# Performance work log

Hardware: AMD Instinct MI355X
Metric: run time of the kernel (lower is better)

## Reference

```python
import jax, jax.numpy as jnp
import numpy as np

N_ATOMS = 100000
BOX = 12.0
NS = 128            # 2**ceil(log2(2*(2*pi/mesh_spacing)*BOX/(2*pi) + 1)) with mesh_spacing=0.2
ORDER = 4           # interpolation_order (cubic)
SMEARING = 1.0      # atomic_gaussian_width
N_SPECIES = 2


def _weights_1d(x):
    # P3M order-4 assignment weights; offsets x in [-1/2, 1/2]
    x2 = x * x
    x3 = x2 * x
    return jnp.stack([
        (1.0 - 6.0 * x + 12.0 * x2 - 8.0 * x3) / 48.0,
        (23.0 - 30.0 * x - 12.0 * x2 + 24.0 * x3) / 48.0,
        (23.0 + 30.0 * x - 12.0 * x2 - 24.0 * x3) / 48.0,
        (1.0 + 6.0 * x + 12.0 * x2 + 8.0 * x3) / 48.0,
    ])  # (ORDER, n_atoms, 3)


def _interpolation(positions, cell, ns):
    # fractional coordinates scaled by mesh size; even order -> offset vs cell midpoint
    inv_cell = jnp.linalg.inv(cell)
    pos_rel = ns * (positions @ inv_cell)                     # (n, 3)
    base = jnp.floor(pos_rel)
    offsets = pos_rel - (base + 0.5)                          # in [-1/2, 1/2)
    w = _weights_1d(offsets)                                  # (4, n, 3)
    shifts = jnp.arange(1 - (ORDER + 1) // 2, 1 + ORDER // 2, dtype=jnp.int32)  # [-1,0,1,2]
    idx = (base.astype(jnp.int32)[None, :, :] + shifts[:, None, None]) % ns    # (4, n, 3)
    return w, idx


def _points_to_mesh(w, idx, charges, ns):
    # scatter charges onto the mesh via the separable 4^3 stencil
    n_ch = charges.shape[1]
    mesh = jnp.zeros((n_ch, ns, ns, ns), dtype=charges.dtype)
    cT = charges.T                                            # (n_ch, n)
    for l in range(ORDER):
        for m in range(ORDER):
            for n in range(ORDER):
                ww = w[l, :, 0] * w[m, :, 1] * w[n, :, 2]     # (n_atoms,)
                mesh = mesh.at[:, idx[l, :, 0], idx[m, :, 1], idx[n, :, 2]].add(ww * cT)
    return mesh


def _mesh_to_points(mesh, w, idx):
    # gather the potential back to the atom positions with the same stencil
    pot = jnp.zeros((mesh.shape[0], w.shape[1]), dtype=mesh.dtype)
    for l in range(ORDER):
        for m in range(ORDER):
            for n in range(ORDER):
                ww = w[l, :, 0] * w[m, :, 1] * w[n, :, 2]
                pot = pot + ww * mesh[:, idx[l, :, 0], idx[m, :, 1], idx[n, :, 2]]
    return pot.T  # (n_atoms, n_ch)


def _fourier_space_convolution(mesh, cell, ns, smearing):
    # Coulomb kernel (potential_exponent=1) with Gaussian smearing, k=0 term removed
    m1 = jnp.fft.fftfreq(ns) * ns                             # integer frequencies
    m3 = jnp.fft.rfftfreq(ns) * ns
    mx, my, mz = jnp.meshgrid(m1, m1, m3, indexing="ij")
    mvec = jnp.stack([mx, my, mz], axis=-1)                   # (ns, ns, ns//2+1, 3)
    k = 2.0 * jnp.pi * (mvec @ jnp.linalg.inv(cell).T)        # reciprocal vectors
    ksq = jnp.sum(k * k, axis=-1)
    safe = jnp.where(ksq > 0.0, ksq, 1.0)
    G = jnp.where(ksq > 0.0, 4.0 * jnp.pi * jnp.exp(-0.5 * smearing * smearing * ksq) / safe, 0.0)
    mesh_hat = jnp.fft.rfftn(mesh, axes=(1, 2, 3))            # unnormalized forward
    pot = jnp.fft.irfftn(mesh_hat * G, s=(ns, ns, ns), axes=(1, 2, 3), norm="forward")
    volume = jnp.abs(jnp.linalg.det(cell))
    return pot / volume


def _compute_single_frame(positions, cell, charges, ns):
    w, idx = _interpolation(positions, cell, ns)
    rho_mesh = _points_to_mesh(w, idx, charges, ns)
    pot_mesh = _fourier_space_convolution(rho_mesh, cell, ns, SMEARING)
    return _mesh_to_points(pot_mesh, w, idx)                  # (n_atoms, n_channels)


def setup_inputs() -> dict:
    key = jax.random.key(0)
    k1, k2 = jax.random.split(key)
    positions = jax.random.uniform(k1, (N_ATOMS, 3), dtype=jnp.float32) * BOX
    cell = BOX * jnp.eye(3, dtype=jnp.float32)
    species = jax.random.randint(k2, (N_ATOMS,), 0, N_SPECIES, dtype=jnp.int32)
    return {"positions": positions, "cell": cell, "species": species, "ns": NS}


def reference(positions, cell, species, ns):
    # compute(): one-hot species channels, then particle-mesh Ewald potential per channel
    charges = jax.nn.one_hot(species, N_SPECIES, dtype=positions.dtype)
    return _compute_single_frame(positions, cell, charges, ns)
```

## Files before the change

### kernel.cpp

```cpp
#include <hip/hip_runtime.h>

#define NSZ 128
#define NS3 (NSZ * NSZ * NSZ)
#define NBUCK_D 16
#define NBUCK (NBUCK_D * NBUCK_D * NBUCK_D)
#define REG 11
#define REG3 (REG * REG * REG)
#define LROW 129
#define LDS_BYTES (NSZ * LROW * sizeof(float2))


__device__ __forceinline__ void inv3x3(const float* __restrict__ c, float* inv) {
    float a00 = c[0], a01 = c[1], a02 = c[2];
    float a10 = c[3], a11 = c[4], a12 = c[5];
    float a20 = c[6], a21 = c[7], a22 = c[8];
    float det = a00 * (a11 * a22 - a12 * a21)
              - a01 * (a10 * a22 - a12 * a20)
              + a02 * (a10 * a21 - a11 * a20);
    float id = 1.0f / det;
    inv[0] = (a11 * a22 - a12 * a21) * id;
    inv[1] = (a02 * a21 - a01 * a22) * id;
    inv[2] = (a01 * a12 - a02 * a11) * id;
    inv[3] = (a12 * a20 - a10 * a22) * id;
    inv[4] = (a00 * a22 - a02 * a20) * id;
    inv[5] = (a02 * a10 - a00 * a12) * id;
    inv[6] = (a10 * a21 - a11 * a20) * id;
    inv[7] = (a01 * a20 - a00 * a21) * id;
    inv[8] = (a00 * a11 - a01 * a10) * id;
}

__device__ __forceinline__ float det3x3(const float* __restrict__ c) {
    return c[0] * (c[4] * c[8] - c[5] * c[7])
         - c[1] * (c[3] * c[8] - c[5] * c[6])
         + c[2] * (c[3] * c[7] - c[4] * c[6]);
}

__device__ __forceinline__ int brev7(int i) { return (int)(__brev((unsigned)i) >> 25); }

__device__ __forceinline__ float2 cadd(float2 a, float2 b) { return make_float2(a.x + b.x, a.y + b.y); }
__device__ __forceinline__ float2 csub(float2 a, float2 b) { return make_float2(a.x - b.x, a.y - b.y); }
__device__ __forceinline__ float2 cmul(float2 a, float2 b) {
    return make_float2(a.x * b.x - a.y * b.y, a.x * b.y + a.y * b.x);
}
__device__ __forceinline__ float2 cmulc(float2 a, float2 b) {
    return make_float2(a.x * b.x + a.y * b.y, a.y * b.x - a.x * b.y);
}

__device__ __forceinline__ void stencil_raw(const float* __restrict__ pos,
                                            const float* __restrict__ cell,
                                            int a, int base[3], float w[3][4]) {
    float inv[9];
    inv3x3(cell, inv);
    float px = pos[a * 3 + 0], py = pos[a * 3 + 1], pz = pos[a * 3 + 2];
    float pr[3];
    pr[0] = (float)NSZ * (px * inv[0] + py * inv[3] + pz * inv[6]);
    pr[1] = (float)NSZ * (px * inv[1] + py * inv[4] + pz * inv[7]);
    pr[2] = (float)NSZ * (px * inv[2] + py * inv[5] + pz * inv[8]);
#pragma unroll
    for (int d = 0; d < 3; d++) {
        float b = floorf(pr[d]);
        float x = pr[d] - b - 0.5f;
        float x2 = x * x, x3 = x2 * x;
        w[d][0] = (1.0f - 6.0f * x + 12.0f * x2 - 8.0f * x3) * (1.0f / 48.0f);
        w[d][1] = (23.0f - 30.0f * x - 12.0f * x2 + 24.0f * x3) * (1.0f / 48.0f);
        w[d][2] = (23.0f + 30.0f * x - 12.0f * x2 - 24.0f * x3) * (1.0f / 48.0f);
        w[d][3] = (1.0f + 6.0f * x + 12.0f * x2 + 8.0f * x3) * (1.0f / 48.0f);
        int bi = (int)b;
        base[d] = bi < 0 ? 0 : (bi > NSZ - 1 ? NSZ - 1 : bi);
    }
}


__global__ void bin_hist(const float* __restrict__ pos, const float* __restrict__ cell,
                         int* __restrict__ counts, int* __restrict__ ba, int n_atoms) {
    int a = blockIdx.x * blockDim.x + threadIdx.x;
    if (a >= n_atoms) return;
    int base[3];
    float w[3][4];
    stencil_raw(pos, cell, a, base, w);
    int bucket = ((base[0] >> 3) * NBUCK_D + (base[1] >> 3)) * NBUCK_D + (base[2] >> 3);
    ba[a] = bucket;
    atomicAdd(&counts[bucket], 1);
}

__global__ void __launch_bounds__(1024)
scan4096(const int* __restrict__ counts, int* __restrict__ starts, int* __restrict__ cursor) {
    __shared__ int sd[1024];
    int t = threadIdx.x;
    int c0 = counts[4 * t], c1 = counts[4 * t + 1], c2 = counts[4 * t + 2], c3 = counts[4 * t + 3];
    int s1 = c0, s2 = c0 + c1, s3 = c0 + c1 + c2, tot = c0 + c1 + c2 + c3;
    sd[t] = tot;
    __syncthreads();
    for (int off = 1; off < 1024; off <<= 1) {
        int v = (t >= off) ? sd[t - off] : 0;
        __syncthreads();
        sd[t] += v;
        __syncthreads();
    }
    int ex = sd[t] - tot;
    starts[4 * t]     = ex;      cursor[4 * t]     = ex;
    starts[4 * t + 1] = ex + s1; cursor[4 * t + 1] = ex + s1;
    starts[4 * t + 2] = ex + s2; cursor[4 * t + 2] = ex + s2;
    starts[4 * t + 3] = ex + s3; cursor[4 * t + 3] = ex + s3;
    if (t == 1023) starts[4096] = sd[1023];
}

__global__ void bin_permute(const int* __restrict__ ba, int* __restrict__ cursor,
                            int* __restrict__ perm, int n_atoms) {
    int a = blockIdx.x * blockDim.x + threadIdx.x;
    if (a >= n_atoms) return;
    int p = atomicAdd(&cursor[ba[a]], 1);
    perm[p] = a;
}


__global__ void __launch_bounds__(256)
scatter_binned(const float* __restrict__ pos, const float* __restrict__ cell,
               const int* __restrict__ species, const int* __restrict__ starts,
               const int* __restrict__ perm, float2* __restrict__ mesh,
               int cx, int cy, int cz) {
    __shared__ float acc[REG3 * 2];
    int bx = blockIdx.x * 2 + cx, by = blockIdx.y * 2 + cy, bz = blockIdx.z * 2 + cz;
    int bucket = (bx * NBUCK_D + by) * NBUCK_D + bz;
    int s = starts[bucket], e = starts[bucket + 1];
    if (s == e) return;
    int t = threadIdx.x;
    for (int i = t; i < REG3 * 2; i += 256) acc[i] = 0.0f;
    __syncthreads();

    int sub = t & 3;
    for (int i = s + (t >> 2); i < e; i += 64) {
        int a = perm[i];
        int base[3];
        float w[3][4];
        stencil_raw(pos, cell, a, base, w);
        int sp = species[a] & 1;
        int rx = base[0] - bx * 8 + sub;
        float wl = w[0][sub];
        int ry0 = base[1] - by * 8;
        int rz0 = base[2] - bz * 8;
#pragma unroll
        for (int m = 0; m < 4; m++) {
            float wlm = wl * w[1][m];
            int rowb = ((rx * REG) + (ry0 + m)) * REG + rz0;
#pragma unroll
            for (int n = 0; n < 4; n++) {
                atomicAdd(&acc[(rowb + n) * 2 + sp], wlm * w[2][n]);
            }
        }
    }
    __syncthreads();

    int ox = bx * 8 - 1, oy = by * 8 - 1, oz = bz * 8 - 1;
    for (int i = t; i < REG3; i += 256) {
        int rx = i / (REG * REG);
        int rem = i % (REG * REG);
        int ry = rem / REG, rz = rem % REG;
        int gx = (ox + rx + NSZ) & (NSZ - 1);
        int gy = (oy + ry + NSZ) & (NSZ - 1);
        int gz = (oz + rz + NSZ) & (NSZ - 1);
        size_t gi = (size_t)(gx * NSZ + gy) * NSZ + gz;
        float2 v = mesh[gi];
        v.x += acc[i * 2];
        v.y += acc[i * 2 + 1];
        mesh[gi] = v;
    }
}


__global__ void scatter_atomic(const float* __restrict__ pos,
                               const float* __restrict__ cell,
                               const int* __restrict__ species,
                               float* __restrict__ meshf, int n_atoms) {
    int a = blockIdx.x * blockDim.x + threadIdx.x;
    if (a >= n_atoms) return;
    int base[3];
    float w[3][4];
    stencil_raw(pos, cell, a, base, w);
    int sp = species[a] & 1;
#pragma unroll
    for (int l = 0; l < 4; l++) {
        int gx = (base[0] + l - 1 + NSZ) & (NSZ - 1);
#pragma unroll
        for (int m = 0; m < 4; m++) {
            int gy = (base[1] + m - 1 + NSZ) & (NSZ - 1);
            float wlm = w[0][l] * w[1][m];
            int rowb = (gx * NSZ + gy) * NSZ;
#pragma unroll
        for (int n = 0; n < 4; n++) {
                int gz = (base[2] + n - 1 + NSZ) & (NSZ - 1);
                atomicAdd(meshf + (((size_t)(rowb + gz)) << 1) + sp, wlm * w[2][n]);
            }
        }
    }
}


__global__ void __launch_bounds__(1024)
fft_fwd_zy(float2* __restrict__ mesh) {
    extern __shared__ float2 sl[];
    __shared__ float2 tw[64];
    int t = threadIdx.x;
    int xs = blockIdx.x;
    if (t < 64) {
        float sn, cs;
        __sincosf(6.283185307179586f * (float)t / 128.0f, &sn, &cs);
        tw[t] = make_float2(cs, -sn);
    }
    const float4* src = (const float4*)(mesh + (size_t)xs * (NSZ * NSZ));
    for (int f = t; f < 8192; f += 1024) {
        float4 v = src[f];
        int y = f >> 6, z = (f & 63) * 2;
        sl[y * LROW + z]     = make_float2(v.x, v.y);
        sl[y * LROW + z + 1] = make_float2(v.z, v.w);
    }
    __syncthreads();
    int lane = t & 127, jb = (t >> 7) * 8;
    for (int s = 6; s >= 0; --s) {
        int half = 1 << s;
        for (int j = jb; j < jb + 8; ++j) {
            int pos = j & (half - 1);
            int i0 = ((j >> s) << (s + 1)) + pos;
            float2 w = tw[pos << (6 - s)];
            float2* p0 = &sl[lane * LROW + i0];
            float2 a = p0[0], b = p0[half];
            p0[0]    = cadd(a, b);
            p0[half] = cmul(csub(a, b), w);
        }
        __syncthreads();
    }
    for (int s = 6; s >= 0; --s) {
        int half = 1 << s;
        for (int j = jb; j < jb + 8; ++j) {
            int pos = j & (half - 1);
            int i0 = ((j >> s) << (s + 1)) + pos;
            float2 w = tw[pos << (6 - s)];
            float2* p0 = &sl[i0 * LROW + lane];
            float2 a = p0[0], b = p0[half * LROW];
            p0[0]           = cadd(a, b);
            p0[half * LROW] = cmul(csub(a, b), w);
        }
        __syncthreads();
    }
    float4* dst = (float4*)(mesh + (size_t)xs * (NSZ * NSZ));
    for (int f = t; f < 8192; f += 1024) {
        int y = f >> 6, z = (f & 63) * 2;
        float2 u0 = sl[y * LROW + z], u1 = sl[y * LROW + z + 1];
        dst[f] = make_float4(u0.x, u0.y, u1.x, u1.y);
    }
}

__global__ void __launch_bounds__(1024)
fft_x_g(float2* __restrict__ mesh, const float* __restrict__ cell, float smearing) {
    extern __shared__ float2 sl[];
    __shared__ float2 tw[64];
    int t = threadIdx.x;
    int y = blockIdx.x;
    if (t < 64) {
        float sn, cs;
        __sincosf(6.283185307179586f * (float)t / 128.0f, &sn, &cs);
        tw[t] = make_float2(cs, -sn);
    }
    for (int f = t; f < 8192; f += 1024) {
        int x = f >> 6, c = f & 63;
        float4 v = ((const float4*)mesh)[(size_t)x * 8192 + (size_t)y * 64 + c];
        int z = c * 2;
        sl[x * LROW + z]     = make_float2(v.x, v.y);
        sl[x * LROW + z + 1] = make_float2(v.z, v.w);
    }
    __syncthreads();
    int lane = t & 127, jb = (t >> 7) * 8;
    for (int s = 6; s >= 0; --s) {
        int half = 1 << s;
        for (int j = jb; j < jb + 8; ++j) {
            int pos = j & (half - 1);
            int i0 = ((j >> s) << (s + 1)) + pos;
            float2 w = tw[pos << (6 - s)];
            float2* p0 = &sl[i0 * LROW + lane];
            float2 a = p0[0], b = p0[half * LROW];
            p0[0]           = cadd(a, b);
            p0[half * LROW] = cmul(csub(a, b), w);
        }
        __syncthreads();
    }
    {
        float inv[9];
        inv3x3(cell, inv);
        float vol = fabsf(det3x3(cell));
        int kyi = brev7(y);
        float fy = (kyi < NSZ / 2) ? (float)kyi : (float)(kyi - NSZ);
        const float twopi = 6.283185307179586f;
        for (int f = t; f < NSZ * NSZ; f += 1024) {
            int px = f >> 7, pz = f & 127;
            int kxi = brev7(px), kzi = brev7(pz);
            float fx = (kxi < NSZ / 2) ? (float)kxi : (float)(kxi - NSZ);
            float fz = (kzi < NSZ / 2) ? (float)kzi : (float)(kzi - NSZ);
            float k0 = twopi * (fx * inv[0] + fy * inv[1] + fz * inv[2]);
            float k1 = twopi * (fx * inv[3] + fy * inv[4] + fz * inv[5]);
            float k2 = twopi * (fx * inv[6] + fy * inv[7] + fz * inv[8]);
            float ksq = k0 * k0 + k1 * k1 + k2 * k2;
            float g = 0.0f;
            if (ksq > 0.0f) {
                g = 12.566370614359172f * __expf(-0.5f * smearing * smearing * ksq) / ksq;
            }
            g /= vol;
            float2 v = sl[px * LROW + pz];
            sl[px * LROW + pz] = make_float2(v.x * g, v.y * g);
        }
    }
    __syncthreads();
    for (int s = 0; s < 7; ++s) {
        int half = 1 << s;
        for (int j = jb; j < jb + 8; ++j) {
            int pos = j & (half - 1);
            int i0 = ((j >> s) << (s + 1)) + pos;
            float2 w = tw[pos << (6 - s)];
            float2* p0 = &sl[i0 * LROW + lane];
            float2 a = p0[0];
            float2 bw = cmulc(p0[half * LROW], w);
            p0[0]           = cadd(a, bw);
            p0[half * LROW] = csub(a, bw);
        }
        __syncthreads();
    }
    for (int f = t; f < 8192; f += 1024) {
        int x = f >> 6, c = f & 63;
        int z = c * 2;
        float2 u0 = sl[x * LROW + z], u1 = sl[x * LROW + z + 1];
        ((float4*)mesh)[(size_t)x * 8192 + (size_t)y * 64 + c] = make_float4(u0.x, u0.y, u1.x, u1.y);
    }
}

__global__ void __launch_bounds__(1024)
fft_inv_yz(float2* __restrict__ mesh) {
    extern __shared__ float2 sl[];
    __shared__ float2 tw[64];
    int t = threadIdx.x;
    int xs = blockIdx.x;
    if (t < 64) {
        float sn, cs;
        __sincosf(6.283185307179586f * (float)t / 128.0f, &sn, &cs);
        tw[t] = make_float2(cs, -sn);
    }
    const float4* src = (const float4*)(mesh + (size_t)xs * (NSZ * NSZ));
    for (int f = t; f < 8192; f += 1024) {
        float4 v = src[f];
        int y = f >> 6, z = (f & 63) * 2;
        sl[y * LROW + z]     = make_float2(v.x, v.y);
        sl[y * LROW + z + 1] = make_float2(v.z, v.w);
    }
    __syncthreads();
    int lane = t & 127, jb = (t >> 7) * 8;
    for (int s = 0; s < 7; ++s) {
        int half = 1 << s;
        for (int j = jb; j < jb + 8; ++j) {
            int pos = j & (half - 1);
            int i0 = ((j >> s) << (s + 1)) + pos;
            float2 w = tw[pos << (6 - s)];
            float2* p0 = &sl[i0 * LROW + lane];
            float2 a = p0[0];
            float2 bw = cmulc(p0[half * LROW], w);
            p0[0]           = cadd(a, bw);
            p0[half * LROW] = csub(a, bw);
        }
        __syncthreads();
    }
    for (int s = 0; s < 7; ++s) {
        int half = 1 << s;
        for (int j = jb; j < jb + 8; ++j) {
            int pos = j & (half - 1);
            int i0 = ((j >> s) << (s + 1)) + pos;
            float2 w = tw[pos << (6 - s)];
            float2* p0 = &sl[lane * LROW + i0];
            float2 a = p0[0];
            float2 bw = cmulc(p0[half], w);
            p0[0]    = cadd(a, bw);
            p0[half] = csub(a, bw);
        }
        __syncthreads();
    }
    float4* dst = (float4*)(mesh + (size_t)xs * (NSZ * NSZ));
    for (int f = t; f < 8192; f += 1024) {
        int y = f >> 6, z = (f & 63) * 2;
        float2 u0 = sl[y * LROW + z], u1 = sl[y * LROW + z + 1];
        dst[f] = make_float4(u0.x, u0.y, u1.x, u1.y);
    }
}


__global__ void gather_kernel(const float* __restrict__ pos,
                              const float* __restrict__ cell,
                              const float2* __restrict__ mesh,
                              const int* __restrict__ perm, int use_perm,
                              float* __restrict__ out,
                              int n_atoms) {
    int i = blockIdx.x * blockDim.x + threadIdx.x;
    if (i >= n_atoms) return;
    int a = use_perm ? perm[i] : i;
    int base[3];
    float w[3][4];
    stencil_raw(pos, cell, a, base, w);
    float acc0 = 0.0f, acc1 = 0.0f;
#pragma unroll
    for (int l = 0; l < 4; l++) {
        int gx = (base[0] + l - 1 + NSZ) & (NSZ - 1);
#pragma unroll
        for (int m = 0; m < 4; m++) {
            int gy = (base[1] + m - 1 + NSZ) & (NSZ - 1);
            float wlm = w[0][l] * w[1][m];
            int rowb = (gx * NSZ + gy) * NSZ;
#pragma unroll
            for (int n = 0; n < 4; n++) {
                int gz = (base[2] + n - 1 + NSZ) & (NSZ - 1);
                float2 v = mesh[rowb + gz];
                float ww = wlm * w[2][n];
                acc0 += ww * v.x;
                acc1 += ww * v.y;
            }
        }
    }
    out[(size_t)a * 2 + 0] = acc0;
    out[(size_t)a * 2 + 1] = acc1;
}


extern "C" void kernel_launch(void* const* d_in, const int* in_sizes, int n_in,
                              void* d_out, int out_size, void* d_ws, size_t ws_size,
                              hipStream_t stream) {
    const float* pos     = (const float*)d_in[0];
    const float* cell    = (const float*)d_in[1];
    const int*   species = (const int*)d_in[2];
    int n_atoms = in_sizes[0] / 3;

    char* ws = (char*)d_ws;
    float2* mesh = (float2*)ws;
    size_t off = (size_t)NS3 * sizeof(float2);
    int* counts = (int*)(ws + off);           off += NBUCK * 4;
    int* starts = (int*)(ws + off);           off += (NBUCK + 4) * 4;
    int* cursor = (int*)(ws + off);           off += NBUCK * 4;
    int* ba     = (int*)(ws + off);           off += (size_t)n_atoms * 4;
    int* perm   = (int*)(ws + off);           off += (size_t)n_atoms * 4;
    bool binned = (ws_size >= off);

    hipFuncSetAttribute((const void*)fft_fwd_zy, hipFuncAttributeMaxDynamicSharedMemorySize, (int)LDS_BYTES);
    hipFuncSetAttribute((const void*)fft_x_g,    hipFuncAttributeMaxDynamicSharedMemorySize, (int)LDS_BYTES);
    hipFuncSetAttribute((const void*)fft_inv_yz, hipFuncAttributeMaxDynamicSharedMemorySize, (int)LDS_BYTES);

    int ab = (n_atoms + 255) / 256;

    if (binned) {
        hipMemsetAsync(ws, 0, (size_t)NS3 * sizeof(float2) + NBUCK * 4, stream);
        bin_hist<<<ab, 256, 0, stream>>>(pos, cell, counts, ba, n_atoms);
        scan4096<<<1, 1024, 0, stream>>>(counts, starts, cursor);
        bin_permute<<<ab, 256, 0, stream>>>(ba, cursor, perm, n_atoms);
        dim3 cg(NBUCK_D / 2, NBUCK_D / 2, NBUCK_D / 2);
        for (int c = 0; c < 8; c++) {
            scatter_binned<<<cg, 256, 0, stream>>>(pos, cell, species, starts, perm,
                                                   mesh, (c >> 2) & 1, (c >> 1) & 1, c & 1);
        }
    } else {
        hipMemsetAsync(mesh, 0, (size_t)NS3 * sizeof(float2), stream);
        scatter_atomic<<<ab, 256, 0, stream>>>(pos, cell, species, (float*)mesh, n_atoms);
    }

    fft_fwd_zy<<<NSZ, 1024, LDS_BYTES, stream>>>(mesh);
    fft_x_g   <<<NSZ, 1024, LDS_BYTES, stream>>>(mesh, cell, 1.0f );
    fft_inv_yz<<<NSZ, 1024, LDS_BYTES, stream>>>(mesh);

    gather_kernel<<<ab, 256, 0, stream>>>(pos, cell, mesh, perm, binned ? 1 : 0,
                                          (float*)d_out, n_atoms);
}
```

Baseline: 285.3 us.

## Replace 8-pass binned scatter with single owner-computes region scatter over sorted records

The scatter now runs in a single launch. Each block owns a disjoint 16^3 mesh region and gathers atoms from the 4x4x4 surrounding buckets into an LDS accumulator, then writes the region directly instead of doing a read-modify-write over halos. Because every mesh cell is written exactly once, the 16MB mesh memset and the eight colored passes are no longer needed. Binning now writes packed float4 records (position, index, species), and gather reads them in sorted order. The scan uses wave shuffles. The cost is redundant stencil work, since each atom is processed by up to eight neighbouring blocks, and a per-atom binary search to locate its record.

```diff
diff --git a/kernel.cpp b/kernel.cpp
--- a/kernel.cpp
+++ b/kernel.cpp
@@ -4,8 +4,8 @@
 #define NS3 (NSZ * NSZ * NSZ)
 #define NBUCK_D 16
 #define NBUCK (NBUCK_D * NBUCK_D * NBUCK_D)
-#define REG 11
-#define REG3 (REG * REG * REG)
+#define RGD 8
+#define RW 16
 #define LROW 129
 #define LDS_BYTES (NSZ * LROW * sizeof(float2))
 
@@ -46,12 +46,9 @@
     return make_float2(a.x * b.x + a.y * b.y, a.y * b.x - a.x * b.y);
 }
 
-__device__ __forceinline__ void stencil_raw(const float* __restrict__ pos,
-                                            const float* __restrict__ cell,
-                                            int a, int base[3], float w[3][4]) {
-    float inv[9];
-    inv3x3(cell, inv);
-    float px = pos[a * 3 + 0], py = pos[a * 3 + 1], pz = pos[a * 3 + 2];
+__device__ __forceinline__ void stencil_pos(float px, float py, float pz,
+                                            const float* __restrict__ inv,
+                                            int base[3], float w[3][4]) {
     float pr[3];
     pr[0] = (float)NSZ * (px * inv[0] + py * inv[3] + pz * inv[6]);
     pr[1] = (float)NSZ * (px * inv[1] + py * inv[4] + pz * inv[7]);
@@ -70,99 +67,156 @@
     }
 }
 
+__device__ __forceinline__ int bucket_of(float px, float py, float pz,
+                                         const float* __restrict__ inv) {
+    float prx = (float)NSZ * (px * inv[0] + py * inv[3] + pz * inv[6]);
+    float pry = (float)NSZ * (px * inv[1] + py * inv[4] + pz * inv[7]);
+    float prz = (float)NSZ * (px * inv[2] + py * inv[5] + pz * inv[8]);
+    int bx = (int)floorf(prx); bx = bx < 0 ? 0 : (bx > NSZ - 1 ? NSZ - 1 : bx);
+    int by = (int)floorf(pry); by = by < 0 ? 0 : (by > NSZ - 1 ? NSZ - 1 : by);
+    int bz = (int)floorf(prz); bz = bz < 0 ? 0 : (bz > NSZ - 1 ? NSZ - 1 : bz);
+    return ((bx >> 3) * NBUCK_D + (by >> 3)) * NBUCK_D + (bz >> 3);
+}
+
 
 __global__ void bin_hist(const float* __restrict__ pos, const float* __restrict__ cell,
-                         int* __restrict__ counts, int* __restrict__ ba, int n_atoms) {
+                         int* __restrict__ counts, int n_atoms) {
     int a = blockIdx.x * blockDim.x + threadIdx.x;
     if (a >= n_atoms) return;
-    int base[3];
-    float w[3][4];
-    stencil_raw(pos, cell, a, base, w);
-    int bucket = ((base[0] >> 3) * NBUCK_D + (base[1] >> 3)) * NBUCK_D + (base[2] >> 3);
-    ba[a] = bucket;
-    atomicAdd(&counts[bucket], 1);
+    float inv[9];
+    inv3x3(cell, inv);
+    atomicAdd(&counts[bucket_of(pos[a * 3], pos[a * 3 + 1], pos[a * 3 + 2], inv)], 1);
 }
 
 __global__ void __launch_bounds__(1024)
 scan4096(const int* __restrict__ counts, int* __restrict__ starts, int* __restrict__ cursor) {
-    __shared__ int sd[1024];
+    __shared__ int wsum[16];
+    __shared__ int wpref[16];
     int t = threadIdx.x;
     int c0 = counts[4 * t], c1 = counts[4 * t + 1], c2 = counts[4 * t + 2], c3 = counts[4 * t + 3];
-    int s1 = c0, s2 = c0 + c1, s3 = c0 + c1 + c2, tot = c0 + c1 + c2 + c3;
-    sd[t] = tot;
-    __syncthreads();
-    for (int off = 1; off < 1024; off <<= 1) {
-        int v = (t >= off) ? sd[t - off] : 0;
-        __syncthreads();
-        sd[t] += v;
-        __syncthreads();
-    }
-    int ex = sd[t] - tot;
-    starts[4 * t]     = ex;      cursor[4 * t]     = ex;
-    starts[4 * t + 1] = ex + s1; cursor[4 * t + 1] = ex + s1;
-    starts[4 * t + 2] = ex + s2; cursor[4 * t + 2] = ex + s2;
-    starts[4 * t + 3] = ex + s3; cursor[4 * t + 3] = ex + s3;
-    if (t == 1023) starts[4096] = sd[1023];
-}
-
-__global__ void bin_permute(const int* __restrict__ ba, int* __restrict__ cursor,
-                            int* __restrict__ perm, int n_atoms) {
+    int tot = c0 + c1 + c2 + c3;
+    int lane = t & 63, w = t >> 6;
+    int incl = tot;
+#pragma unroll
+    for (int o = 1; o < 64; o <<= 1) {
+        int v = __shfl_up(incl, o, 64);
+        if (lane >= o) incl += v;
+    }
+    if (lane == 63) wsum[w] = incl;
+    __syncthreads();
+    if (t < 16) {
+        int v = wsum[t], p = 0;
+        for (int i = 0; i < 16; i++) { if (i < t) p += wsum[i]; }
+        wpref[t] = p;
+        (void)v;
+    }
+    __syncthreads();
+    int ex = wpref[w] + incl - tot;
+    starts[4 * t]     = ex;           cursor[4 * t]     = ex;
+    starts[4 * t + 1] = ex + c0;      cursor[4 * t + 1] = ex + c0;
+    starts[4 * t + 2] = ex + c0 + c1; cursor[4 * t + 2] = ex + c0 + c1;
+    starts[4 * t + 3] = ex + c0 + c1 + c2; cursor[4 * t + 3] = ex + c0 + c1 + c2;
+    if (t == 1023) starts[4096] = ex + tot;
+}
+
+__global__ void bin_permute(const float* __restrict__ pos, const float* __restrict__ cell,
+                            const int* __restrict__ species, int* __restrict__ cursor,
+                            float4* __restrict__ recs, int n_atoms) {
     int a = blockIdx.x * blockDim.x + threadIdx.x;
     if (a >= n_atoms) return;
-    int p = atomicAdd(&cursor[ba[a]], 1);
-    perm[p] = a;
-}
-
+    float inv[9];
+    inv3x3(cell, inv);
+    float px = pos[a * 3], py = pos[a * 3 + 1], pz = pos[a * 3 + 2];
+    int b = bucket_of(px, py, pz, inv);
+    int p = atomicAdd(&cursor[b], 1);
+    recs[p] = make_float4(px, py, pz, __int_as_float((a << 1) | (species[a] & 1)));
+}
+
+
+#define ACC_ROW 33
+#define ACC_SZ (RW * RW * ACC_ROW)
 
 __global__ void __launch_bounds__(256)
-scatter_binned(const float* __restrict__ pos, const float* __restrict__ cell,
-               const int* __restrict__ species, const int* __restrict__ starts,
-               const int* __restrict__ perm, float2* __restrict__ mesh,
-               int cx, int cy, int cz) {
-    __shared__ float acc[REG3 * 2];
-    int bx = blockIdx.x * 2 + cx, by = blockIdx.y * 2 + cy, bz = blockIdx.z * 2 + cz;
-    int bucket = (bx * NBUCK_D + by) * NBUCK_D + bz;
-    int s = starts[bucket], e = starts[bucket + 1];
-    if (s == e) return;
+scatter_region(const float* __restrict__ cell, const int* __restrict__ starts,
+               const float4* __restrict__ recs, float2* __restrict__ mesh) {
+    __shared__ float acc[ACC_SZ];
+    __shared__ int rstart_s[64];
+    __shared__ int rpref_s[64];
+    __shared__ int rtot_s;
     int t = threadIdx.x;
-    for (int i = t; i < REG3 * 2; i += 256) acc[i] = 0.0f;
-    __syncthreads();
-
-    int sub = t & 3;
-    for (int i = s + (t >> 2); i < e; i += 64) {
-        int a = perm[i];
+    int BX = blockIdx.x, BY = blockIdx.y, BZ = blockIdx.z;
+
+    for (int i = t; i < ACC_SZ; i += 256) acc[i] = 0.0f;
+
+    if (t < 64) {
+        int dx = (t >> 4) & 3, dy = (t >> 2) & 3, dz = t & 3;
+        int bx = (2 * BX - 1 + dx) & (NBUCK_D - 1);
+        int by = (2 * BY - 1 + dy) & (NBUCK_D - 1);
+        int bz = (2 * BZ - 1 + dz) & (NBUCK_D - 1);
+        int b = (bx * NBUCK_D + by) * NBUCK_D + bz;
+        int s0 = starts[b];
+        int c = starts[b + 1] - s0;
+        rstart_s[t] = s0;
+        int incl = c;
+#pragma unroll
+        for (int o = 1; o < 64; o <<= 1) {
+            int v = __shfl_up(incl, o, 64);
+            if (t >= o) incl += v;
+        }
+        rpref_s[t] = incl - c;
+        if (t == 63) rtot_s = incl;
+    }
+    __syncthreads();
+
+    float inv[9];
+    inv3x3(cell, inv);
+    int M = rtot_s;
+    int sx = BX << 4, sy = BY << 4, sz = BZ << 4;
+    int lane = t & 63;
+
+    for (int i = t; i < M; i += 256) {
+        int r = 0;
+#pragma unroll
+        for (int step = 32; step; step >>= 1)
+            if (r + step < 64 && rpref_s[r + step] <= i) r += step;
+        float4 rec = recs[rstart_s[r] + (i - rpref_s[r])];
         int base[3];
         float w[3][4];
-        stencil_raw(pos, cell, a, base, w);
-        int sp = species[a] & 1;
-        int rx = base[0] - bx * 8 + sub;
-        float wl = w[0][sub];
-        int ry0 = base[1] - by * 8;
-        int rz0 = base[2] - bz * 8;
-#pragma unroll
-        for (int m = 0; m < 4; m++) {
-            float wlm = wl * w[1][m];
-            int rowb = ((rx * REG) + (ry0 + m)) * REG + rz0;
-#pragma unroll
-            for (int n = 0; n < 4; n++) {
-                atomicAdd(&acc[(rowb + n) * 2 + sp], wlm * w[2][n]);
+        stencil_pos(rec.x, rec.y, rec.z, inv, base, w);
+        int rbx = (base[0] - sx + 2) & (NSZ - 1);
+        int rby = (base[1] - sy + 2) & (NSZ - 1);
+        int rbz = (base[2] - sz + 2) & (NSZ - 1);
+        if (rbx >= 19 || rby >= 19 || rbz >= 19) continue;
+        rbx -= 2; rby -= 2; rbz -= 2;
+        int sp = __float_as_int(rec.w) & 1;
+#pragma unroll
+        for (int l = 0; l < 4; l++) {
+            int cx = rbx + l - 1;
+            if ((unsigned)cx >= (unsigned)RW) continue;
+            float wl = w[0][l];
+#pragma unroll
+            for (int m = 0; m < 4; m++) {
+                int cy = rby + m - 1;
+                if ((unsigned)cy >= (unsigned)RW) continue;
+                float wlm = wl * w[1][m];
+                int rowb = (cx * RW + cy) * ACC_ROW + sp;
+#pragma unroll
+                for (int nn = 0; nn < 4; nn++) {
+                    int n = (nn + lane) & 3;
+                    int cz = rbz + n - 1;
+                    if ((unsigned)cz >= (unsigned)RW) continue;
+                    atomicAdd(&acc[rowb + cz * 2], wlm * w[2][n]);
+                }
             }
         }
     }
     __syncthreads();
 
-    int ox = bx * 8 - 1, oy = by * 8 - 1, oz = bz * 8 - 1;
-    for (int i = t; i < REG3; i += 256) {
-        int rx = i / (REG * REG);
-        int rem = i % (REG * REG);
-        int ry = rem / REG, rz = rem % REG;
-        int gx = (ox + rx + NSZ) & (NSZ - 1);
-        int gy = (oy + ry + NSZ) & (NSZ - 1);
-        int gz = (oz + rz + NSZ) & (NSZ - 1);
-        size_t gi = (size_t)(gx * NSZ + gy) * NSZ + gz;
-        float2 v = mesh[gi];
-        v.x += acc[i * 2];
-        v.y += acc[i * 2 + 1];
+    for (int i = t; i < RW * RW * RW; i += 256) {
+        int x = i >> 8, y = (i >> 4) & 15, z = i & 15;
+        float2 v = make_float2(acc[(x * RW + y) * ACC_ROW + z * 2],
+                               acc[(x * RW + y) * ACC_ROW + z * 2 + 1]);
+        size_t gi = (size_t)((sx + x) * NSZ + (sy + y)) * NSZ + (sz + z);
         mesh[gi] = v;
     }
 }
@@ -174,9 +228,11 @@
                                float* __restrict__ meshf, int n_atoms) {
     int a = blockIdx.x * blockDim.x + threadIdx.x;
     if (a >= n_atoms) return;
+    float inv[9];
+    inv3x3(cell, inv);
     int base[3];
     float w[3][4];
-    stencil_raw(pos, cell, a, base, w);
+    stencil_pos(pos[a * 3], pos[a * 3 + 1], pos[a * 3 + 2], inv, base, w);
     int sp = species[a] & 1;
 #pragma unroll
     for (int l = 0; l < 4; l++) {
@@ -187,7 +243,7 @@
             float wlm = w[0][l] * w[1][m];
             int rowb = (gx * NSZ + gy) * NSZ;
 #pragma unroll
-        for (int n = 0; n < 4; n++) {
+            for (int n = 0; n < 4; n++) {
                 int gz = (base[2] + n - 1 + NSZ) & (NSZ - 1);
                 atomicAdd(meshf + (((size_t)(rowb + gz)) << 1) + sp, wlm * w[2][n]);
             }
@@ -388,18 +444,18 @@
 }
 
 
-__global__ void gather_kernel(const float* __restrict__ pos,
-                              const float* __restrict__ cell,
+__global__ void gather_sorted(const float* __restrict__ cell,
                               const float2* __restrict__ mesh,
-                              const int* __restrict__ perm, int use_perm,
-                              float* __restrict__ out,
-                              int n_atoms) {
+                              const float4* __restrict__ recs,
+                              float2* __restrict__ out, int n_atoms) {
     int i = blockIdx.x * blockDim.x + threadIdx.x;
     if (i >= n_atoms) return;
-    int a = use_perm ? perm[i] : i;
+    float4 rec = recs[i];
+    float inv[9];
+    inv3x3(cell, inv);
     int base[3];
     float w[3][4];
-    stencil_raw(pos, cell, a, base, w);
+    stencil_pos(rec.x, rec.y, rec.z, inv, base, w);
     float acc0 = 0.0f, acc1 = 0.0f;
 #pragma unroll
     for (int l = 0; l < 4; l++) {
@@ -419,8 +475,40 @@
             }
         }
     }
-    out[(size_t)a * 2 + 0] = acc0;
-    out[(size_t)a * 2 + 1] = acc1;
+    out[__float_as_int(rec.w) >> 1] = make_float2(acc0, acc1);
+}
+
+__global__ void gather_plain(const float* __restrict__ pos,
+                             const float* __restrict__ cell,
+                             const float2* __restrict__ mesh,
+                             float2* __restrict__ out, int n_atoms) {
+    int a = blockIdx.x * blockDim.x + threadIdx.x;
+    if (a >= n_atoms) return;
+    float inv[9];
+    inv3x3(cell, inv);
+    int base[3];
+    float w[3][4];
+    stencil_pos(pos[a * 3], pos[a * 3 + 1], pos[a * 3 + 2], inv, base, w);
+    float acc0 = 0.0f, acc1 = 0.0f;
+#pragma unroll
+    for (int l = 0; l < 4; l++) {
+        int gx = (base[0] + l - 1 + NSZ) & (NSZ - 1);
+#pragma unroll
+        for (int m = 0; m < 4; m++) {
+            int gy = (base[1] + m - 1 + NSZ) & (NSZ - 1);
+            float wlm = w[0][l] * w[1][m];
+            int rowb = (gx * NSZ + gy) * NSZ;
+#pragma unroll
+            for (int n = 0; n < 4; n++) {
+                int gz = (base[2] + n - 1 + NSZ) & (NSZ - 1);
+                float2 v = mesh[rowb + gz];
+                float ww = wlm * w[2][n];
+                acc0 += ww * v.x;
+                acc1 += ww * v.y;
+            }
+        }
+    }
+    out[a] = make_float2(acc0, acc1);
 }
 
 
@@ -438,8 +526,8 @@
     int* counts = (int*)(ws + off);           off += NBUCK * 4;
     int* starts = (int*)(ws + off);           off += (NBUCK + 4) * 4;
     int* cursor = (int*)(ws + off);           off += NBUCK * 4;
-    int* ba     = (int*)(ws + off);           off += (size_t)n_atoms * 4;
-    int* perm   = (int*)(ws + off);           off += (size_t)n_atoms * 4;
+    off = (off + 15) & ~(size_t)15;
+    float4* recs = (float4*)(ws + off);       off += (size_t)n_atoms * 16;
     bool binned = (ws_size >= off);
 
     hipFuncSetAttribute((const void*)fft_fwd_zy, hipFuncAttributeMaxDynamicSharedMemorySize, (int)LDS_BYTES);
@@ -449,15 +537,12 @@
     int ab = (n_atoms + 255) / 256;
 
     if (binned) {
-        hipMemsetAsync(ws, 0, (size_t)NS3 * sizeof(float2) + NBUCK * 4, stream);
-        bin_hist<<<ab, 256, 0, stream>>>(pos, cell, counts, ba, n_atoms);
+        hipMemsetAsync(counts, 0, NBUCK * 4, stream);
+        bin_hist<<<ab, 256, 0, stream>>>(pos, cell, counts, n_atoms);
         scan4096<<<1, 1024, 0, stream>>>(counts, starts, cursor);
-        bin_permute<<<ab, 256, 0, stream>>>(ba, cursor, perm, n_atoms);
-        dim3 cg(NBUCK_D / 2, NBUCK_D / 2, NBUCK_D / 2);
-        for (int c = 0; c < 8; c++) {
-            scatter_binned<<<cg, 256, 0, stream>>>(pos, cell, species, starts, perm,
-                                                   mesh, (c >> 2) & 1, (c >> 1) & 1, c & 1);
-        }
+        bin_permute<<<ab, 256, 0, stream>>>(pos, cell, species, cursor, recs, n_atoms);
+        dim3 rg(RGD, RGD, RGD);
+        scatter_region<<<rg, 256, 0, stream>>>(cell, starts, recs, mesh);
     } else {
         hipMemsetAsync(mesh, 0, (size_t)NS3 * sizeof(float2), stream);
         scatter_atomic<<<ab, 256, 0, stream>>>(pos, cell, species, (float*)mesh, n_atoms);
@@ -467,6 +552,9 @@
     fft_x_g   <<<NSZ, 1024, LDS_BYTES, stream>>>(mesh, cell, 1.0f );
     fft_inv_yz<<<NSZ, 1024, LDS_BYTES, stream>>>(mesh);
 
-    gather_kernel<<<ab, 256, 0, stream>>>(pos, cell, mesh, perm, binned ? 1 : 0,
-                                          (float*)d_out, n_atoms);
-}
+    if (binned) {
+        gather_sorted<<<ab, 256, 0, stream>>>(cell, mesh, recs, (float2*)d_out, n_atoms);
+    } else {
+        gather_plain<<<ab, 256, 0, stream>>>(pos, cell, mesh, (float2*)d_out, n_atoms);
+    }
+}
```

Result: faster. 246.2 us (-13.7%).
